# Kernel tuning notes

Measured on AMD Instinct MI355X. Metric: run time of the kernel, lower is better.

## Reference

```python
import jax, jax.numpy as jnp
import numpy as np

EPS = 1e-6  # SublayerConnection LayerNorm eps (annotated-transformer style)
NEG = -1e9
NUM_USED = 3  # used_domain_list = ['news','book','iwslt'] -> mask indices 0,1,2


def _layer_norm(x, scale, bias):
    m = jnp.mean(x, axis=-1, keepdims=True)
    v = jnp.mean(jnp.square(x - m), axis=-1, keepdims=True)
    return (x - m) * jax.lax.rsqrt(v + EPS) * scale + bias


def setup_inputs() -> dict:
    key = jax.random.key(0)
    ks = jax.random.split(key, 8)
    B, L, H, F, D = 8, 1024, 1024, 2048, 4
    s = 0.02
    return {
        "x": jax.random.normal(ks[0], (B, L, H), jnp.float32),
        "domain_mask": jnp.array([1, 1, 1, 0], jnp.int32),
        "gate_w1": jax.random.normal(ks[1], (H, D), jnp.float32) * s,
        "gate_b1": jnp.zeros((D,), jnp.float32),
        "gate_w2": jax.random.normal(ks[2], (D, D), jnp.float32) * s,
        "gate_b2": jnp.zeros((D,), jnp.float32),
        "ln_s_book": jnp.ones((H,), jnp.float32),
        "ln_b_book": jnp.zeros((H,), jnp.float32),
        "ln_s_iwslt": jnp.ones((H,), jnp.float32),
        "ln_b_iwslt": jnp.zeros((H,), jnp.float32),
        "ad_w1": jax.random.normal(ks[3], (H, F), jnp.float32) * s,
        "ad_b1": jnp.zeros((F,), jnp.float32),
        "ad_w2": jax.random.normal(ks[4], (F, H), jnp.float32) * s,
        "ad_b2": jnp.zeros((H,), jnp.float32),
    }


def reference(x, domain_mask, gate_w1, gate_b1, gate_w2, gate_b2,
              ln_s_book, ln_b_book, ln_s_iwslt, ln_b_iwslt,
              ad_w1, ad_b1, ad_w2, ad_b2):
    # inner gate for target_domain='book': Linear -> ReLU -> Linear, masked softmax
    h = jnp.maximum(jnp.einsum('blh,hd->bld', x, gate_w1) + gate_b1, 0.0)
    logits = jnp.einsum('bld,de->ble', h, gate_w2) + gate_b2          # [B,L,Dmax]
    logits = jnp.where(domain_mask == 0, NEG, logits)
    prob = jax.nn.softmax(logits, axis=-1)
    weights = prob[..., :NUM_USED]                                     # [B,L,3]

    # per-domain wo_residual adapter (dropout identity at eval).
    # Faithful quirk: both domains use target_domain ('book') adapter weights,
    # but each domain's own SublayerConnection LayerNorm params.
    def adapt(ln_s, ln_b):
        z = _layer_norm(x, ln_s, ln_b)
        z = jnp.maximum(jnp.einsum('blh,hf->blf', z, ad_w1) + ad_b1, 0.0)
        return jnp.einsum('blf,fh->blh', z, ad_w2) + ad_b2

    outs = jnp.stack([x, adapt(ln_s_book, ln_b_book),
                      adapt(ln_s_iwslt, ln_b_iwslt)], axis=-1)         # [B,L,H,3]
    mix = jnp.einsum('blhd,bld->blh', outs, weights)
    return x + mix
```

## Files before the change

### kernel.cpp

```cpp
#include <hip/hip_runtime.h>
#include <stdint.h>

typedef __attribute__((ext_vector_type(8))) short bf16x8;
typedef __attribute__((ext_vector_type(4))) float f32x4;

__device__ __forceinline__ unsigned short f2bf(float f) {
  union { float f; unsigned u; } v; v.f = f;
  unsigned r = v.u + 0x7fffu + ((v.u >> 16) & 1u);
  return (unsigned short)(r >> 16);
}
__device__ __forceinline__ float bf2f(unsigned short u) {
  union { unsigned u; float f; } v; v.u = ((unsigned)u) << 16; return v.f;
}
__device__ __forceinline__ void gload16(const void* g, void* l) {
  __builtin_amdgcn_global_load_lds(
      (const __attribute__((address_space(1))) unsigned int*)(uintptr_t)g,
      (__attribute__((address_space(3))) unsigned int*)(uintptr_t)l,
      16, 0, 0);
}

__global__ __launch_bounds__(256)
void k_gate_ln(const float* __restrict__ x, const int* __restrict__ dmask,
               const float* __restrict__ gw1, const float* __restrict__ gb1,
               const float* __restrict__ gw2, const float* __restrict__ gb2,
               const float* __restrict__ sb, const float* __restrict__ bb,
               const float* __restrict__ si, const float* __restrict__ bi,
               float* __restrict__ wout,
               unsigned short* __restrict__ z)
{
  const int lane = threadIdx.x & 63;
  const int row = blockIdx.x * 4 + (threadIdx.x >> 6);
  const float* xr = x + (size_t)row * 1024;

  float4 xv[4];
  float p0 = 0.f, p1 = 0.f, p2 = 0.f, p3 = 0.f, s = 0.f, ss = 0.f;
#pragma unroll
  for (int j = 0; j < 4; ++j) {
    const int i0 = lane * 4 + j * 256;
    xv[j] = *(const float4*)(xr + i0);
    const float xc[4] = {xv[j].x, xv[j].y, xv[j].z, xv[j].w};
#pragma unroll
    for (int c = 0; c < 4; ++c) {
      const float4 w = *(const float4*)(gw1 + (size_t)(i0 + c) * 4);
      p0 += xc[c] * w.x; p1 += xc[c] * w.y; p2 += xc[c] * w.z; p3 += xc[c] * w.w;
      s += xc[c]; ss += xc[c] * xc[c];
    }
  }
#pragma unroll
  for (int m = 32; m >= 1; m >>= 1) {
    p0 += __shfl_xor(p0, m, 64); p1 += __shfl_xor(p1, m, 64);
    p2 += __shfl_xor(p2, m, 64); p3 += __shfl_xor(p3, m, 64);
    s  += __shfl_xor(s,  m, 64); ss += __shfl_xor(ss, m, 64);
  }
  const float h0 = fmaxf(p0 + gb1[0], 0.f), h1 = fmaxf(p1 + gb1[1], 0.f);
  const float h2 = fmaxf(p2 + gb1[2], 0.f), h3 = fmaxf(p3 + gb1[3], 0.f);
  float lg[4];
#pragma unroll
  for (int e = 0; e < 4; ++e) {
    float val = h0 * gw2[e] + h1 * gw2[4 + e] + h2 * gw2[8 + e] + h3 * gw2[12 + e] + gb2[e];
    lg[e] = (dmask[e] == 0) ? -1.0e9f : val;
  }
  const float mx = fmaxf(fmaxf(lg[0], lg[1]), fmaxf(lg[2], lg[3]));
  const float e0 = expf(lg[0] - mx), e1 = expf(lg[1] - mx);
  const float e2 = expf(lg[2] - mx), e3 = expf(lg[3] - mx);
  const float inv = 1.f / (e0 + e1 + e2 + e3);
  if (lane == 0) {
    float4 wv; wv.x = e0 * inv; wv.y = e1 * inv; wv.z = e2 * inv; wv.w = 0.f;
    *(float4*)(wout + (size_t)row * 4) = wv;
  }
  const float mean = s * (1.f / 1024.f);
  const float rstd = rsqrtf(ss * (1.f / 1024.f) - mean * mean + 1e-6f);

#pragma unroll
  for (int j = 0; j < 4; ++j) {
    const int i0 = lane * 4 + j * 256;
    const float4 sbv = *(const float4*)(sb + i0);
    const float4 bbv = *(const float4*)(bb + i0);
    const float4 siv = *(const float4*)(si + i0);
    const float4 biv = *(const float4*)(bi + i0);
    const float xc[4] = {xv[j].x, xv[j].y, xv[j].z, xv[j].w};
    const float sbs[4] = {sbv.x, sbv.y, sbv.z, sbv.w};
    const float bbs[4] = {bbv.x, bbv.y, bbv.z, bbv.w};
    const float sis[4] = {siv.x, siv.y, siv.z, siv.w};
    const float bis[4] = {biv.x, biv.y, biv.z, biv.w};
    ushort4 zb, zi;
    unsigned short zbv[4], ziv[4];
#pragma unroll
    for (int c = 0; c < 4; ++c) {
      const float xn = (xc[c] - mean) * rstd;
      zbv[c] = f2bf(xn * sbs[c] + bbs[c]);
      ziv[c] = f2bf(xn * sis[c] + bis[c]);
    }
    zb.x = zbv[0]; zb.y = zbv[1]; zb.z = zbv[2]; zb.w = zbv[3];
    zi.x = ziv[0]; zi.y = ziv[1]; zi.z = ziv[2]; zi.w = ziv[3];
    *(ushort4*)(z + (size_t)(2 * row) * 1024 + i0) = zb;
    *(ushort4*)(z + (size_t)(2 * row + 1) * 1024 + i0) = zi;
  }
}

__global__ __launch_bounds__(256)
void k_transpose_bf16(const float* __restrict__ src, unsigned short* __restrict__ dst,
                      int R, int C)
{
  __shared__ float tile[32][33];
  const int tx = threadIdx.x & 31, ty = threadIdx.x >> 5;
  const int c0 = blockIdx.x * 32, r0 = blockIdx.y * 32;
#pragma unroll
  for (int j = 0; j < 32; j += 8)
    tile[ty + j][tx] = src[(size_t)(r0 + ty + j) * C + c0 + tx];
  __syncthreads();
#pragma unroll
  for (int j = 0; j < 32; j += 8)
    dst[(size_t)(c0 + ty + j) * R + r0 + tx] = f2bf(tile[tx][ty + j]);
}

#define LOADA(dst, q) do {                                                            \
  dst[0][0] = *(const bf16x8*)(curA + (arowB + (2*(q)+0)*16) * 128 + koff0);          \
  dst[0][1] = *(const bf16x8*)(curA + (arowB + (2*(q)+0)*16) * 128 + koff1);          \
  dst[1][0] = *(const bf16x8*)(curA + (arowB + (2*(q)+1)*16) * 128 + koff0);          \
  dst[1][1] = *(const bf16x8*)(curA + (arowB + (2*(q)+1)*16) * 128 + koff1);          \
} while (0)

#define MFMAQ(src, q) do {                                                            \
  __builtin_amdgcn_s_setprio(1);                                                      \
  _Pragma("unroll")                                                                   \
  for (int i = 0; i < 2; ++i) {                                                       \
    _Pragma("unroll")                                                                 \
    for (int ni = 0; ni < 4; ++ni) {                                                  \
      acc[2*(q)+i][ni] = __builtin_amdgcn_mfma_f32_16x16x32_bf16(src[i][0], bf[ni][0], acc[2*(q)+i][ni], 0, 0, 0); \
      acc[2*(q)+i][ni] = __builtin_amdgcn_mfma_f32_16x16x32_bf16(src[i][1], bf[ni][1], acc[2*(q)+i][ni], 0, 0, 0); \
    } }                                                                               \
  __builtin_amdgcn_s_setprio(0);                                                      \
} while (0)

template <int MODE, int K, int NBX>
__global__ __launch_bounds__(512, 2)
void gemm256(const unsigned short* __restrict__ A,
             const unsigned short* __restrict__ Bt,
             const float* __restrict__ bias,
             unsigned short* __restrict__ Cb,
             const float* __restrict__ x,
             const float* __restrict__ wgt,
             float* __restrict__ outp)
{
  constexpr int NKT = K / 64;
  constexpr int N = NBX * 256;
  __shared__ __align__(16) char lds[131072];

  const int tid = threadIdx.x;
  const int wave = tid >> 6, lane = tid & 63;
  const int lr = lane & 15, lk = lane >> 4;
  const int wm = wave >> 2, wn = wave & 3;

  const int cpx = (int)gridDim.x >> 3;
  const int flat = (int)blockIdx.x;
  const int swz = (flat & 7) * cpx + (flat >> 3);
  const int bm0 = (swz / NBX) * 256;
  const int bn0 = (swz % NBX) * 256;

  const int srow = tid >> 3;
  const int schunk = ((tid & 7) ^ (srow & 7)) * 8;
  const unsigned short* aSrc = A + (size_t)(bm0 + srow) * K + schunk;
  const unsigned short* bSrc = Bt + (size_t)(bn0 + srow) * K + schunk;
  const int ldsWaveOff = wave * 1024;

  const int xorv = (lr & 7) << 4;
  const int koff0 = (lk * 16) ^ xorv;
  const int koff1 = (64 + lk * 16) ^ xorv;
  const int arowB = wm * 128 + lr;
  const int browB = wn * 64 + lr;

  f32x4 acc[8][4] = {};

  auto stage_tile = [&](int tt) {
#pragma unroll
    for (int h = 0; h < 4; ++h) {
      const unsigned short* sp = (h < 2 ? bSrc : aSrc) + (size_t)((h & 1) * 128) * K + tt * 64;
      char* d = lds + ((tt & 1) << 16) + ((h < 2) ? 32768 : 0) + ((h & 1) << 14) + ldsWaveOff;
      gload16(sp, d);
      gload16(sp + (size_t)64 * K, d + 8192);
    }
  };

  stage_tile(0);
  asm volatile("s_waitcnt vmcnt(0)" ::: "memory");
  __builtin_amdgcn_s_barrier();

#pragma unroll 2
  for (int t = 0; t < NKT; ++t) {
    const char* curA = lds + ((t & 1) << 16);
    const char* curB = curA + 32768;
    if (t + 1 < NKT) stage_tile(t + 1);

    bf16x8 bf[4][2];
#pragma unroll
    for (int ni = 0; ni < 4; ++ni) {
      bf[ni][0] = *(const bf16x8*)(curB + (browB + ni * 16) * 128 + koff0);
      bf[ni][1] = *(const bf16x8*)(curB + (browB + ni * 16) * 128 + koff1);
    }
    bf16x8 a0[2][2], a1[2][2];
    LOADA(a0, 0);
    LOADA(a1, 1);
    MFMAQ(a0, 0);  LOADA(a0, 2);
    MFMAQ(a1, 1);  LOADA(a1, 3);
    MFMAQ(a0, 2);
    MFMAQ(a1, 3);

    asm volatile("s_waitcnt vmcnt(0)" ::: "memory");
    __builtin_amdgcn_s_barrier();
  }

  __syncthreads();

  if (MODE == 0) {
#pragma unroll
    for (int ni = 0; ni < 4; ++ni) {
      const int colb = (wn * 64 + ni * 16 + lr) * 2;
      const float bv = bias[bn0 + wn * 64 + ni * 16 + lr];
#pragma unroll
      for (int mi = 0; mi < 8; ++mi) {
#pragma unroll
        for (int j = 0; j < 4; ++j) {
          const int row = wm * 128 + mi * 16 + lk * 4 + j;
          float v = fmaxf(acc[mi][ni][j] + bv, 0.f);
          *(unsigned short*)(lds + row * 512 + (colb ^ ((row & 7) << 4))) = f2bf(v);
        }
      }
    }
    __syncthreads();
#pragma unroll
    for (int sx = 0; sx < 16; ++sx) {
      const int row = wave * 32 + sx * 2 + (lane >> 5);
      const int c = lane & 31;
      bf16x8 vv = *(const bf16x8*)(lds + row * 512 + ((c * 16) ^ ((row & 7) << 4)));
      *(bf16x8*)(Cb + (size_t)(bm0 + row) * N + bn0 + c * 8) = vv;
    }
  } else {
    const int orbase = bm0 >> 1;
#pragma unroll
    for (int mi = 0; mi < 8; ++mi) {
      const int lr0 = wm * 64 + mi * 8 + lk * 2;
      const float4 wa = *(const float4*)(wgt + (size_t)(orbase + lr0) * 4);
      const float4 wb = *(const float4*)(wgt + (size_t)(orbase + lr0 + 1) * 4);
#pragma unroll
      for (int ni = 0; ni < 4; ++ni) {
        const int colb = (wn * 64 + ni * 16 + lr) * 4;
        const float bv = bias[bn0 + wn * 64 + ni * 16 + lr];
        float m0 = wa.y * (acc[mi][ni][0] + bv) + wa.z * (acc[mi][ni][1] + bv);
        float m1 = wb.y * (acc[mi][ni][2] + bv) + wb.z * (acc[mi][ni][3] + bv);
        *(float*)(lds + (size_t)lr0 * 1024 + (colb ^ ((lr0 & 6) << 5))) = m0;
        *(float*)(lds + (size_t)(lr0 + 1) * 1024 + (colb ^ (((lr0 + 1) & 6) << 5))) = m1;
      }
    }
    __syncthreads();
#pragma unroll
    for (int sx = 0; sx < 16; ++sx) {
      const int lrow = wave * 16 + sx;
      const int gor = orbase + lrow;
      f32x4 m = *(const f32x4*)(lds + (size_t)lrow * 1024 + ((lane * 16) ^ ((lrow & 6) << 5)));
      const float4 xv = *(const float4*)(x + (size_t)gor * 1024 + bn0 + lane * 4);
      const float w0 = wgt[(size_t)gor * 4];
      f32x4 o;
      o[0] = xv.x * (1.f + w0) + m[0];
      o[1] = xv.y * (1.f + w0) + m[1];
      o[2] = xv.z * (1.f + w0) + m[2];
      o[3] = xv.w * (1.f + w0) + m[3];
      *(f32x4*)(outp + (size_t)gor * 1024 + bn0 + lane * 4) = o;
    }
  }
}

extern "C" void kernel_launch(void* const* d_in, const int* in_sizes, int n_in,
                              void* d_out, int out_size, void* d_ws, size_t ws_size,
                              hipStream_t stream) {
  const float* x    = (const float*)d_in[0];
  const int*   dm   = (const int*)  d_in[1];
  const float* gw1  = (const float*)d_in[2];
  const float* gb1  = (const float*)d_in[3];
  const float* gw2  = (const float*)d_in[4];
  const float* gb2  = (const float*)d_in[5];
  const float* lsb  = (const float*)d_in[6];
  const float* lbb  = (const float*)d_in[7];
  const float* lsi  = (const float*)d_in[8];
  const float* lbi  = (const float*)d_in[9];
  const float* aw1  = (const float*)d_in[10];
  const float* ab1  = (const float*)d_in[11];
  const float* aw2  = (const float*)d_in[12];
  const float* ab2  = (const float*)d_in[13];
  float* out = (float*)d_out;

  char* ws = (char*)d_ws;
  float*          wgt  = (float*)(ws + 0);
  unsigned short* z    = (unsigned short*)(ws + 131072);
  unsigned short* w1t  = (unsigned short*)(ws + 131072 + 33554432);
  unsigned short* w2t  = (unsigned short*)(ws + 131072 + 33554432 + 4194304);
  unsigned short* hbuf = (unsigned short*)(ws + 131072 + 33554432 + 8388608);

  k_gate_ln<<<2048, 256, 0, stream>>>(x, dm, gw1, gb1, gw2, gb2,
                                      lsb, lbb, lsi, lbi, wgt, z);
  k_transpose_bf16<<<dim3(2048/32, 1024/32), 256, 0, stream>>>(aw1, w1t, 1024, 2048);
  k_transpose_bf16<<<dim3(1024/32, 2048/32), 256, 0, stream>>>(aw2, w2t, 2048, 1024);
  gemm256<0, 1024, 8><<<512, 512, 0, stream>>>(z, w1t, ab1, hbuf, nullptr, nullptr, nullptr);
  gemm256<1, 2048, 4><<<256, 512, 0, stream>>>(hbuf, w2t, ab2, nullptr, x, wgt, out);
}
```

Baseline: 258.8 us.

## Use 16 waves per 256x256 GEMM tile with smaller per-wave subtiles

The GEMM kernel now runs 1024 threads (16 waves) per block instead of 512. Each wave computes a 64x64 subtile with 4x4 accumulators instead of 128x64 with 8x4, and staging and epilogue work is split across twice as many threads. The K-step is split into two half-K phases that load fragments and then issue MFMAs. This cuts per-wave register pressure and adds more waves to hide latency, but the same 128KB of LDS per block still limits residency, and each wave does less reuse of fragments and pipelines fewer loads.

```diff
diff --git a/kernel.cpp b/kernel.cpp
--- a/kernel.cpp
+++ b/kernel.cpp
@@ -114,27 +114,8 @@
     dst[(size_t)(c0 + ty + j) * R + r0 + tx] = f2bf(tile[tx][ty + j]);
 }
 
-#define LOADA(dst, q) do {                                                            \
-  dst[0][0] = *(const bf16x8*)(curA + (arowB + (2*(q)+0)*16) * 128 + koff0);          \
-  dst[0][1] = *(const bf16x8*)(curA + (arowB + (2*(q)+0)*16) * 128 + koff1);          \
-  dst[1][0] = *(const bf16x8*)(curA + (arowB + (2*(q)+1)*16) * 128 + koff0);          \
-  dst[1][1] = *(const bf16x8*)(curA + (arowB + (2*(q)+1)*16) * 128 + koff1);          \
-} while (0)
-
-#define MFMAQ(src, q) do {                                                            \
-  __builtin_amdgcn_s_setprio(1);                                                      \
-  _Pragma("unroll")                                                                   \
-  for (int i = 0; i < 2; ++i) {                                                       \
-    _Pragma("unroll")                                                                 \
-    for (int ni = 0; ni < 4; ++ni) {                                                  \
-      acc[2*(q)+i][ni] = __builtin_amdgcn_mfma_f32_16x16x32_bf16(src[i][0], bf[ni][0], acc[2*(q)+i][ni], 0, 0, 0); \
-      acc[2*(q)+i][ni] = __builtin_amdgcn_mfma_f32_16x16x32_bf16(src[i][1], bf[ni][1], acc[2*(q)+i][ni], 0, 0, 0); \
-    } }                                                                               \
-  __builtin_amdgcn_s_setprio(0);                                                      \
-} while (0)
-
 template <int MODE, int K, int NBX>
-__global__ __launch_bounds__(512, 2)
+__global__ __launch_bounds__(1024, 4)
 void gemm256(const unsigned short* __restrict__ A,
              const unsigned short* __restrict__ Bt,
              const float* __restrict__ bias,
@@ -162,23 +143,21 @@
   const int schunk = ((tid & 7) ^ (srow & 7)) * 8;
   const unsigned short* aSrc = A + (size_t)(bm0 + srow) * K + schunk;
   const unsigned short* bSrc = Bt + (size_t)(bn0 + srow) * K + schunk;
-  const int ldsWaveOff = wave * 1024;
 
   const int xorv = (lr & 7) << 4;
   const int koff0 = (lk * 16) ^ xorv;
   const int koff1 = (64 + lk * 16) ^ xorv;
-  const int arowB = wm * 128 + lr;
-  const int browB = wn * 64 + lr;
-
-  f32x4 acc[8][4] = {};
+  const int arow = wm * 64 + lr;
+  const int brow = wn * 64 + lr;
+
+  f32x4 acc[4][4] = {};
 
   auto stage_tile = [&](int tt) {
-#pragma unroll
-    for (int h = 0; h < 4; ++h) {
-      const unsigned short* sp = (h < 2 ? bSrc : aSrc) + (size_t)((h & 1) * 128) * K + tt * 64;
-      char* d = lds + ((tt & 1) << 16) + ((h < 2) ? 32768 : 0) + ((h & 1) << 14) + ldsWaveOff;
-      gload16(sp, d);
-      gload16(sp + (size_t)64 * K, d + 8192);
+    char* dbase = lds + ((tt & 1) << 16);
+#pragma unroll
+    for (int r = 0; r < 2; ++r) {
+      gload16(aSrc + (size_t)(r * 128) * K + tt * 64, dbase + r * 16384 + wave * 1024);
+      gload16(bSrc + (size_t)(r * 128) * K + tt * 64, dbase + 32768 + r * 16384 + wave * 1024);
     }
   };
 
@@ -192,19 +171,33 @@
     const char* curB = curA + 32768;
     if (t + 1 < NKT) stage_tile(t + 1);
 
-    bf16x8 bf[4][2];
-#pragma unroll
-    for (int ni = 0; ni < 4; ++ni) {
-      bf[ni][0] = *(const bf16x8*)(curB + (browB + ni * 16) * 128 + koff0);
-      bf[ni][1] = *(const bf16x8*)(curB + (browB + ni * 16) * 128 + koff1);
-    }
-    bf16x8 a0[2][2], a1[2][2];
-    LOADA(a0, 0);
-    LOADA(a1, 1);
-    MFMAQ(a0, 0);  LOADA(a0, 2);
-    MFMAQ(a1, 1);  LOADA(a1, 3);
-    MFMAQ(a0, 2);
-    MFMAQ(a1, 3);
+    bf16x8 bfr[4], afr[4];
+#pragma unroll
+    for (int ni = 0; ni < 4; ++ni)
+      bfr[ni] = *(const bf16x8*)(curB + (brow + ni * 16) * 128 + koff0);
+#pragma unroll
+    for (int mi = 0; mi < 4; ++mi)
+      afr[mi] = *(const bf16x8*)(curA + (arow + mi * 16) * 128 + koff0);
+    __builtin_amdgcn_s_setprio(1);
+#pragma unroll
+    for (int mi = 0; mi < 4; ++mi)
+#pragma unroll
+      for (int ni = 0; ni < 4; ++ni)
+        acc[mi][ni] = __builtin_amdgcn_mfma_f32_16x16x32_bf16(afr[mi], bfr[ni], acc[mi][ni], 0, 0, 0);
+    __builtin_amdgcn_s_setprio(0);
+#pragma unroll
+    for (int ni = 0; ni < 4; ++ni)
+      bfr[ni] = *(const bf16x8*)(curB + (brow + ni * 16) * 128 + koff1);
+#pragma unroll
+    for (int mi = 0; mi < 4; ++mi)
+      afr[mi] = *(const bf16x8*)(curA + (arow + mi * 16) * 128 + koff1);
+    __builtin_amdgcn_s_setprio(1);
+#pragma unroll
+    for (int mi = 0; mi < 4; ++mi)
+#pragma unroll
+      for (int ni = 0; ni < 4; ++ni)
+        acc[mi][ni] = __builtin_amdgcn_mfma_f32_16x16x32_bf16(afr[mi], bfr[ni], acc[mi][ni], 0, 0, 0);
+    __builtin_amdgcn_s_setprio(0);
 
     asm volatile("s_waitcnt vmcnt(0)" ::: "memory");
     __builtin_amdgcn_s_barrier();
@@ -215,22 +208,22 @@
   if (MODE == 0) {
 #pragma unroll
     for (int ni = 0; ni < 4; ++ni) {
-      const int colb = (wn * 64 + ni * 16 + lr) * 2;
-      const float bv = bias[bn0 + wn * 64 + ni * 16 + lr];
-#pragma unroll
-      for (int mi = 0; mi < 8; ++mi) {
+      const int col = wn * 64 + ni * 16 + lr;
+      const float bv = bias[bn0 + col];
+#pragma unroll
+      for (int mi = 0; mi < 4; ++mi) {
 #pragma unroll
         for (int j = 0; j < 4; ++j) {
-          const int row = wm * 128 + mi * 16 + lk * 4 + j;
+          const int row = wm * 64 + mi * 16 + lk * 4 + j;
           float v = fmaxf(acc[mi][ni][j] + bv, 0.f);
-          *(unsigned short*)(lds + row * 512 + (colb ^ ((row & 7) << 4))) = f2bf(v);
+          *(unsigned short*)(lds + row * 512 + ((col * 2) ^ ((row & 7) << 4))) = f2bf(v);
         }
       }
     }
     __syncthreads();
 #pragma unroll
-    for (int sx = 0; sx < 16; ++sx) {
-      const int row = wave * 32 + sx * 2 + (lane >> 5);
+    for (int sx = 0; sx < 8; ++sx) {
+      const int row = wave * 16 + sx * 2 + (lane >> 5);
       const int c = lane & 31;
       bf16x8 vv = *(const bf16x8*)(lds + row * 512 + ((c * 16) ^ ((row & 7) << 4)));
       *(bf16x8*)(Cb + (size_t)(bm0 + row) * N + bn0 + c * 8) = vv;
@@ -238,8 +231,8 @@
   } else {
     const int orbase = bm0 >> 1;
 #pragma unroll
-    for (int mi = 0; mi < 8; ++mi) {
-      const int lr0 = wm * 64 + mi * 8 + lk * 2;
+    for (int mi = 0; mi < 4; ++mi) {
+      const int lr0 = wm * 32 + mi * 8 + lk * 2;
       const float4 wa = *(const float4*)(wgt + (size_t)(orbase + lr0) * 4);
       const float4 wb = *(const float4*)(wgt + (size_t)(orbase + lr0 + 1) * 4);
 #pragma unroll
@@ -254,8 +247,8 @@
     }
     __syncthreads();
 #pragma unroll
-    for (int sx = 0; sx < 16; ++sx) {
-      const int lrow = wave * 16 + sx;
+    for (int sx = 0; sx < 8; ++sx) {
+      const int lrow = wave * 8 + sx;
       const int gor = orbase + lrow;
       f32x4 m = *(const f32x4*)(lds + (size_t)lrow * 1024 + ((lane * 16) ^ ((lrow & 6) << 5)));
       const float4 xv = *(const float4*)(x + (size_t)gor * 1024 + bn0 + lane * 4);
@@ -300,6 +293,6 @@
                                       lsb, lbb, lsi, lbi, wgt, z);
   k_transpose_bf16<<<dim3(2048/32, 1024/32), 256, 0, stream>>>(aw1, w1t, 1024, 2048);
   k_transpose_bf16<<<dim3(1024/32, 2048/32), 256, 0, stream>>>(aw2, w2t, 2048, 1024);
-  gemm256<0, 1024, 8><<<512, 512, 0, stream>>>(z, w1t, ab1, hbuf, nullptr, nullptr, nullptr);
-  gemm256<1, 2048, 4><<<256, 512, 0, stream>>>(hbuf, w2t, ab2, nullptr, x, wgt, out);
-}
+  gemm256<0, 1024, 8><<<512, 1024, 0, stream>>>(z, w1t, ab1, hbuf, nullptr, nullptr, nullptr);
+  gemm256<1, 2048, 4><<<256, 1024, 0, stream>>>(hbuf, w2t, ab2, nullptr, x, wgt, out);
+}
```

Measured after the change: 299.7 us. +15.8%, slower.
